# Kernel tuning notes

Hardware: AMD Instinct MI355X
Metric: run time of the kernel (lower is better)

The kernel has to match this reference:

```python
import jax, jax.numpy as jnp
import numpy as np

K = 3          # kernel size
STRIDE = 1
PAD = 1        # dilation*(K-1)//2
DIL = 1


def _bilinear_gather(x, py, px):
    """Bilinear sample x[B,C,H,W] at float coords (py,px) of shape [B,K2,Ho,Wo].
    Out-of-bounds contributions are zero (matches detectron2 DeformConv).
    Returns [B,C,K2,Ho,Wo]."""
    B, C, H, W = x.shape
    xf = x.reshape(B, C, H * W)
    y0 = jnp.floor(py)
    x0 = jnp.floor(px)
    out = jnp.zeros((B, C) + py.shape[1:], dtype=x.dtype)
    gather = jax.vmap(lambda xb, ib: xb[:, ib])  # ([C,HW],[K2,Ho,Wo])->[C,K2,Ho,Wo]
    for cy, cx in ((y0, x0), (y0, x0 + 1.0), (y0 + 1.0, x0), (y0 + 1.0, x0 + 1.0)):
        wgt = (1.0 - jnp.abs(py - cy)) * (1.0 - jnp.abs(px - cx))
        valid = (cy >= 0) & (cy <= H - 1) & (cx >= 0) & (cx <= W - 1)
        yi = jnp.clip(cy, 0, H - 1).astype(jnp.int32)
        xi = jnp.clip(cx, 0, W - 1).astype(jnp.int32)
        idx = yi * W + xi  # [B,K2,Ho,Wo]
        vals = gather(xf, idx)  # [B,C,K2,Ho,Wo]
        out = out + (wgt * valid.astype(x.dtype))[:, None] * vals
    return out


def _deform_conv(x, offset, weight):
    B, C, H, W = x.shape
    Ho = (H + 2 * PAD - (DIL * (K - 1) + 1)) // STRIDE + 1
    Wo = (W + 2 * PAD - (DIL * (K - 1) + 1)) // STRIDE + 1
    K2 = K * K
    # base sampling grid
    hs = (jnp.arange(Ho) * STRIDE - PAD).astype(x.dtype)  # [Ho]
    ws = (jnp.arange(Wo) * STRIDE - PAD).astype(x.dtype)  # [Wo]
    ky, kx = jnp.meshgrid(jnp.arange(K), jnp.arange(K), indexing='ij')
    ky = (ky.reshape(-1) * DIL).astype(x.dtype)  # [K2], row-major taps
    kx = (kx.reshape(-1) * DIL).astype(x.dtype)
    # offsets: channel 2k = dy, 2k+1 = dx for tap k
    off = offset.reshape(B, K2, 2, Ho, Wo)
    dy, dx = off[:, :, 0], off[:, :, 1]  # [B,K2,Ho,Wo]
    py = hs[None, None, :, None] + ky[None, :, None, None] + dy
    px = ws[None, None, None, :] + kx[None, :, None, None] + dx
    sampled = _bilinear_gather(x, py, px)  # [B,C,K2,Ho,Wo]
    wk = weight.reshape(weight.shape[0], C, K2)  # groups=1
    return jnp.einsum('ocK,bcKhw->bohw', wk, sampled)


def setup_inputs() -> dict:
    key = jax.random.key(0)
    k1, k2, k3 = jax.random.split(key, 3)
    B, C, H, W = 8, 256, 64, 64
    x = jax.random.normal(k1, (B, C, H, W), dtype=jnp.float32)
    offset = jax.random.normal(k2, (B, 2 * K * K, H, W), dtype=jnp.float32)
    weight = jax.random.normal(k3, (256, C, K, K), dtype=jnp.float32) * 0.02
    return {"x": x, "offset": offset, "weight": weight}


def reference(x, offset, weight):
    return _deform_conv(x, offset, weight)
```

## Files before the change

### kernel.cpp

```cpp
#include <hip/hip_runtime.h>
#include <stdint.h>


#define Bb 8
#define Cc 256
#define Hh 64
#define Ww 64
#define Pp 4096
#define Oo 256
#define NK2 9
#define NPAIR 36
#define BN 64
#define SROW 40
#define WT_BYTES (2u * 72u * 256u * 32u)

typedef __attribute__((ext_vector_type(4))) float f32x4;
typedef __attribute__((ext_vector_type(8))) short s16x8;
typedef __attribute__((ext_vector_type(4))) int   i32x4;

static __device__ __forceinline__ unsigned short f2bf(float f) {
    union { float f; uint32_t u; } v; v.f = f;
    return (unsigned short)((v.u + 0x7fffu + ((v.u >> 16) & 1u)) >> 16);
}
static __device__ __forceinline__ int imin(int a, int b) { return a < b ? a : b; }
static __device__ __forceinline__ int imax(int a, int b) { return a > b ? a : b; }

__global__ void prep_weight(const float* __restrict__ w, unsigned short* __restrict__ wt) {
    __shared__ unsigned short Lw[8][2304];
    int o0 = blockIdx.x * 8, tid = threadIdx.x;
    for (int r = 0; r < 8; r++)
        for (int i = tid; i < 2304; i += 256)
            Lw[r][i] = f2bf(w[(o0 + r) * 2304 + i]);
    __syncthreads();
    int r = tid >> 5, c32 = tid & 31;
    for (int ks = 0; ks < 72; ks++) {
        int c = (ks & 7) * 32 + c32, k2 = ks >> 3;
        wt[ks * 8192 + (o0 + r) * 32 + c32] = Lw[r][c * 9 + k2];
    }
}

__global__ void prep_x(const float* __restrict__ x, unsigned short* __restrict__ xt) {
    __shared__ unsigned short t[64][65];
    int b = blockIdx.z, c0 = blockIdx.y * 64, p0 = blockIdx.x * 64;
    int tl = threadIdx.x & 63, tg = threadIdx.x >> 6;
    #pragma unroll
    for (int r = 0; r < 16; r++) {
        int cr = r * 4 + tg;
        t[cr][tl] = f2bf(x[((size_t)(b * Cc + c0 + cr) * Pp) + p0 + tl]);
    }
    __syncthreads();
    #pragma unroll
    for (int r = 0; r < 16; r++) {
        int pr = r * 4 + tg;
        xt[((size_t)(b * Pp + p0 + pr) * Cc) + c0 + tl] = t[tl][pr];
    }
}

__global__ __launch_bounds__(512, 4)
void dcn_main(const float* __restrict__ off, const unsigned short* __restrict__ wt,
              const unsigned short* __restrict__ xt, float* __restrict__ out) {
    __shared__ __align__(16) unsigned short Sl[2][2][BN][SROW];
    __shared__ __align__(16) int   tidx[NK2][BN][4];
    __shared__ __align__(16) float twgt[NK2][BN][4];

    const int b   = blockIdx.x & 7;
    const int p0  = (blockIdx.x >> 3) * BN;
    const int tid = threadIdx.x;
    const int lane = tid & 63;
    const int wv   = tid >> 6;
    const int quad = lane >> 4;
    const int l16  = lane & 15;
    const int moff = wv * 32;

    const int px  = tid >> 3;
    const int sub = tid & 7;
    const int hh_ = sub >> 2;
    const int cc_ = (sub & 3) * 8;

    const char* xtb = (const char*)xt + (size_t)b * Pp * Cc * 2;

    for (int t = tid; t < NK2 * BN; t += 512) {
        int k2 = t >> 6, pxl = t & 63;
        int pl = p0 + pxl;
        int hh = pl >> 6, ww = pl & 63;
        int ky = k2 / 3, kx = k2 - ky * 3;
        float dy = off[((size_t)(b * 18 + 2 * k2    ) * Pp) + pl];
        float dx = off[((size_t)(b * 18 + 2 * k2 + 1) * Pp) + pl];
        float py  = (float)(hh - 1 + ky) + dy;
        float pxf = (float)(ww - 1 + kx) + dx;
        float y0f = floorf(py), x0f = floorf(pxf);
        int   y0 = (int)y0f,  x0 = (int)x0f;
        int   y1 = y0 + 1,    x1 = x0 + 1;
        float ly = py - y0f,  lx = pxf - x0f;
        float oy = 1.f - ly,  ox = 1.f - lx;
        bool vy0 = (y0 >= 0) && (y0 < Hh);
        bool vy1 = (y1 >= 0) && (y1 < Hh);
        bool vx0 = (x0 >= 0) && (x0 < Ww);
        bool vx1 = (x1 >= 0) && (x1 < Ww);
        int cy0 = imin(imax(y0, 0), Hh - 1), cy1 = imin(imax(y1, 0), Hh - 1);
        int cx0 = imin(imax(x0, 0), Ww - 1), cx1 = imin(imax(x1, 0), Ww - 1);
        tidx[k2][pxl][0] = (cy0 * Ww + cx0) * 512;  twgt[k2][pxl][0] = (vy0 && vx0) ? oy * ox : 0.f;
        tidx[k2][pxl][1] = (cy0 * Ww + cx1) * 512;  twgt[k2][pxl][1] = (vy0 && vx1) ? oy * lx : 0.f;
        tidx[k2][pxl][2] = (cy1 * Ww + cx0) * 512;  twgt[k2][pxl][2] = (vy1 && vx0) ? ly * ox : 0.f;
        tidx[k2][pxl][3] = (cy1 * Ww + cx1) * 512;  twgt[k2][pxl][3] = (vy1 && vx1) ? ly * lx : 0.f;
    }
    __syncthreads();

    int   tio[4];
    float twv[4];
    {
        i32x4 ti = *(const i32x4*)&tidx[0][px][0];
        f32x4 tw = *(const f32x4*)&twgt[0][px][0];
        #pragma unroll
        for (int t = 0; t < 4; t++) { tio[t] = ti[t]; twv[t] = tw[t]; }
    }

    auto sample_into = [&](int pr) {
        int coff = (pr & 3) * 128 + sub * 16;
        float s[8];
        #pragma unroll
        for (int j = 0; j < 8; j++) s[j] = 0.f;
        #pragma unroll
        for (int t = 0; t < 4; t++) {
            uint4 v = *(const uint4*)(xtb + tio[t] + coff);
            float wg = twv[t];
            s[0] += wg * __uint_as_float(v.x << 16);
            s[1] += wg * __uint_as_float(v.x & 0xffff0000u);
            s[2] += wg * __uint_as_float(v.y << 16);
            s[3] += wg * __uint_as_float(v.y & 0xffff0000u);
            s[4] += wg * __uint_as_float(v.z << 16);
            s[5] += wg * __uint_as_float(v.z & 0xffff0000u);
            s[6] += wg * __uint_as_float(v.w << 16);
            s[7] += wg * __uint_as_float(v.w & 0xffff0000u);
        }
        uint4 d;
        d.x = __builtin_amdgcn_perm(__float_as_uint(s[1]), __float_as_uint(s[0]), 0x07060302u);
        d.y = __builtin_amdgcn_perm(__float_as_uint(s[3]), __float_as_uint(s[2]), 0x07060302u);
        d.z = __builtin_amdgcn_perm(__float_as_uint(s[5]), __float_as_uint(s[4]), 0x07060302u);
        d.w = __builtin_amdgcn_perm(__float_as_uint(s[7]), __float_as_uint(s[6]), 0x07060302u);
        *(uint4*)&Sl[pr & 1][hh_][px][cc_] = d;
    };

    f32x4 acc[2][4];
    #pragma unroll
    for (int mt = 0; mt < 2; mt++)
        #pragma unroll
        for (int nt = 0; nt < 4; nt++) acc[mt][nt] = (f32x4){0.f, 0.f, 0.f, 0.f};

    sample_into(0);

    for (int pr = 0; pr < NPAIR; pr++) {
        __syncthreads();

        const char* wb = (const char*)wt + ((size_t)pr << 15);
        s16x8 af[2][2];
        #pragma unroll
        for (int h = 0; h < 2; h++)
            #pragma unroll
            for (int mt = 0; mt < 2; mt++)
                af[h][mt] = *(const s16x8*)(wb + h * 16384 +
                                            (moff + mt * 16 + l16) * 64 + quad * 16);

        int prn = pr + 1;
        if (prn < NPAIR) {
            if ((prn & 3) == 0) {
                int k2 = prn >> 2;
                i32x4 ti = *(const i32x4*)&tidx[k2][px][0];
                f32x4 tw = *(const f32x4*)&twgt[k2][px][0];
                #pragma unroll
                for (int t = 0; t < 4; t++) { tio[t] = ti[t]; twv[t] = tw[t]; }
            }
            sample_into(prn);
        }

        #pragma unroll
        for (int h = 0; h < 2; h++) {
            s16x8 bfr[4];
            #pragma unroll
            for (int nt = 0; nt < 4; nt++)
                bfr[nt] = *(const s16x8*)&Sl[pr & 1][h][nt * 16 + l16][quad * 8];
            #pragma unroll
            for (int mt = 0; mt < 2; mt++)
                #pragma unroll
                for (int nt = 0; nt < 4; nt++)
                    acc[mt][nt] = __builtin_amdgcn_mfma_f32_16x16x32_bf16(
                        af[h][mt], bfr[nt], acc[mt][nt], 0, 0, 0);
        }
    }

    float* op = out + ((size_t)b * Oo) * Pp + p0;
    #pragma unroll
    for (int mt = 0; mt < 2; mt++)
        #pragma unroll
        for (int nt = 0; nt < 4; nt++)
            #pragma unroll
            for (int r = 0; r < 4; r++) {
                int o_ = moff + mt * 16 + quad * 4 + r;
                int p_ = nt * 16 + l16;
                op[(size_t)o_ * Pp + p_] = acc[mt][nt][r];
            }
}

extern "C" void kernel_launch(void* const* d_in, const int* in_sizes, int n_in,
                              void* d_out, int out_size, void* d_ws, size_t ws_size,
                              hipStream_t stream) {
    (void)in_sizes; (void)n_in; (void)out_size; (void)ws_size;
    const float* x   = (const float*)d_in[0];
    const float* off = (const float*)d_in[1];
    const float* w   = (const float*)d_in[2];
    float* out = (float*)d_out;

    unsigned short* wt = (unsigned short*)d_ws;
    unsigned short* xt = (unsigned short*)((char*)d_ws + WT_BYTES);

    hipLaunchKernelGGL(prep_weight, dim3(32), dim3(256), 0, stream, w, wt);
    hipLaunchKernelGGL(prep_x, dim3(64, 4, 8), dim3(256), 0, stream, x, xt);
    hipLaunchKernelGGL(dcn_main, dim3(512), dim3(512), 0, stream, off, wt, xt, out);
}
```

Before: 165.7 us.

## Merge prep kernels and software-pipeline gathers and weight loads across MFMA

The two preprocessing kernels are fused into one launch. The x transpose now uses vectorized float4 reads and a swizzled LDS tile with 16-byte stores, and the weight prep uses 4-output blocks spread over more blocks. In the main kernel, the global gathers and weight-fragment loads for the next step are issued before the current step's MFMAs, and the bilinear reduction runs after them. Weight fragments are double-buffered in registers, which hides load latency but raises register pressure. The mask on odd bf16 lanes is also dropped, accepting tiny low-bit errors.

```diff
diff --git a/kernel.cpp b/kernel.cpp
--- a/kernel.cpp
+++ b/kernel.cpp
@@ -25,34 +25,54 @@
 static __device__ __forceinline__ int imin(int a, int b) { return a < b ? a : b; }
 static __device__ __forceinline__ int imax(int a, int b) { return a > b ? a : b; }
 
-__global__ void prep_weight(const float* __restrict__ w, unsigned short* __restrict__ wt) {
-    __shared__ unsigned short Lw[8][2304];
-    int o0 = blockIdx.x * 8, tid = threadIdx.x;
-    for (int r = 0; r < 8; r++)
-        for (int i = tid; i < 2304; i += 256)
-            Lw[r][i] = f2bf(w[(o0 + r) * 2304 + i]);
-    __syncthreads();
-    int r = tid >> 5, c32 = tid & 31;
-    for (int ks = 0; ks < 72; ks++) {
-        int c = (ks & 7) * 32 + c32, k2 = ks >> 3;
-        wt[ks * 8192 + (o0 + r) * 32 + c32] = Lw[r][c * 9 + k2];
-    }
-}
-
-__global__ void prep_x(const float* __restrict__ x, unsigned short* __restrict__ xt) {
-    __shared__ unsigned short t[64][65];
-    int b = blockIdx.z, c0 = blockIdx.y * 64, p0 = blockIdx.x * 64;
-    int tl = threadIdx.x & 63, tg = threadIdx.x >> 6;
-    #pragma unroll
-    for (int r = 0; r < 16; r++) {
-        int cr = r * 4 + tg;
-        t[cr][tl] = f2bf(x[((size_t)(b * Cc + c0 + cr) * Pp) + p0 + tl]);
-    }
-    __syncthreads();
-    #pragma unroll
-    for (int r = 0; r < 16; r++) {
-        int pr = r * 4 + tg;
-        xt[((size_t)(b * Pp + p0 + pr) * Cc) + c0 + tl] = t[tl][pr];
+__global__ __launch_bounds__(256)
+void prep(const float* __restrict__ x, const float* __restrict__ w,
+          unsigned short* __restrict__ xt, unsigned short* __restrict__ wt) {
+    __shared__ __align__(16) unsigned short L[9216];
+    const int bx = blockIdx.x, tid = threadIdx.x;
+
+    if (bx < 2048) {
+        unsigned short (*t2)[72] = (unsigned short(*)[72])L;
+        const int b = bx & 7, ti = bx >> 3;
+        const int c0 = (ti & 3) * 64, p0 = (ti >> 2) * 64;
+        #pragma unroll
+        for (int rd = 0; rd < 4; rd++) {
+            int c = (tid >> 4) + rd * 16;
+            int px4 = (tid & 15) * 4;
+            f32x4 fv = *(const f32x4*)&x[(size_t)(b * Cc + c0 + c) * Pp + p0 + px4];
+            #pragma unroll
+            for (int j = 0; j < 4; j++) {
+                int px = px4 + j;
+                int chunk = ((c >> 3) + px) & 7;
+                t2[px][chunk * 8 + (c & 7)] = f2bf(fv[j]);
+            }
+        }
+        __syncthreads();
+        #pragma unroll
+        for (int rd = 0; rd < 2; rd++) {
+            int px = (tid >> 3) + rd * 32;
+            int k = tid & 7;
+            int chunk = (k + px) & 7;
+            uint4 u = *(const uint4*)&t2[px][chunk * 8];
+            *(uint4*)&xt[(size_t)(b * Pp + p0 + px) * Cc + c0 + k * 8] = u;
+        }
+    } else {
+        const int o0 = (bx - 2048) * 4;
+        #pragma unroll
+        for (int r9 = 0; r9 < 9; r9++) {
+            int idx = r9 * 256 + tid;
+            f32x4 fv = *(const f32x4*)&w[(size_t)o0 * 2304 + (size_t)idx * 4];
+            #pragma unroll
+            for (int j = 0; j < 4; j++) L[idx * 4 + j] = f2bf(fv[j]);
+        }
+        __syncthreads();
+        #pragma unroll 4
+        for (int i = 0; i < 36; i++) {
+            int ks = i * 2 + (tid >> 7);
+            int r = (tid >> 5) & 3, c32 = tid & 31;
+            int c = (ks & 7) * 32 + c32, k2 = ks >> 3;
+            wt[(size_t)ks * 8192 + (o0 + r) * 32 + c32] = L[r * 2304 + c * 9 + k2];
+        }
     }
 }
 
@@ -108,6 +128,7 @@
 
     int   tio[4];
     float twv[4];
+    uint4 g[4];
     {
         i32x4 ti = *(const i32x4*)&tidx[0][px][0];
         f32x4 tw = *(const f32x4*)&twgt[0][px][0];
@@ -115,53 +136,40 @@
         for (int t = 0; t < 4; t++) { tio[t] = ti[t]; twv[t] = tw[t]; }
     }
 
-    auto sample_into = [&](int pr) {
-        int coff = (pr & 3) * 128 + sub * 16;
-        float s[8];
-        #pragma unroll
-        for (int j = 0; j < 8; j++) s[j] = 0.f;
-        #pragma unroll
-        for (int t = 0; t < 4; t++) {
-            uint4 v = *(const uint4*)(xtb + tio[t] + coff);
-            float wg = twv[t];
-            s[0] += wg * __uint_as_float(v.x << 16);
-            s[1] += wg * __uint_as_float(v.x & 0xffff0000u);
-            s[2] += wg * __uint_as_float(v.y << 16);
-            s[3] += wg * __uint_as_float(v.y & 0xffff0000u);
-            s[4] += wg * __uint_as_float(v.z << 16);
-            s[5] += wg * __uint_as_float(v.z & 0xffff0000u);
-            s[6] += wg * __uint_as_float(v.w << 16);
-            s[7] += wg * __uint_as_float(v.w & 0xffff0000u);
-        }
-        uint4 d;
-        d.x = __builtin_amdgcn_perm(__float_as_uint(s[1]), __float_as_uint(s[0]), 0x07060302u);
-        d.y = __builtin_amdgcn_perm(__float_as_uint(s[3]), __float_as_uint(s[2]), 0x07060302u);
-        d.z = __builtin_amdgcn_perm(__float_as_uint(s[5]), __float_as_uint(s[4]), 0x07060302u);
-        d.w = __builtin_amdgcn_perm(__float_as_uint(s[7]), __float_as_uint(s[6]), 0x07060302u);
-        *(uint4*)&Sl[pr & 1][hh_][px][cc_] = d;
-    };
-
     f32x4 acc[2][4];
     #pragma unroll
     for (int mt = 0; mt < 2; mt++)
         #pragma unroll
         for (int nt = 0; nt < 4; nt++) acc[mt][nt] = (f32x4){0.f, 0.f, 0.f, 0.f};
 
-    sample_into(0);
-
-    for (int pr = 0; pr < NPAIR; pr++) {
+    auto reduce_store = [&](int prn) {
+        float s0 = 0.f, s1 = 0.f, s2 = 0.f, s3 = 0.f, s4 = 0.f, s5 = 0.f, s6 = 0.f, s7 = 0.f;
+        #pragma unroll
+        for (int t = 0; t < 4; t++) {
+            uint4 v = g[t];
+            float wg = twv[t];
+            s0 += wg * __uint_as_float(v.x << 16);
+            s1 += wg * __uint_as_float(v.x);
+            s2 += wg * __uint_as_float(v.y << 16);
+            s3 += wg * __uint_as_float(v.y);
+            s4 += wg * __uint_as_float(v.z << 16);
+            s5 += wg * __uint_as_float(v.z);
+            s6 += wg * __uint_as_float(v.w << 16);
+            s7 += wg * __uint_as_float(v.w);
+        }
+        uint4 d;
+        d.x = __builtin_amdgcn_perm(__float_as_uint(s1), __float_as_uint(s0), 0x07060302u);
+        d.y = __builtin_amdgcn_perm(__float_as_uint(s3), __float_as_uint(s2), 0x07060302u);
+        d.z = __builtin_amdgcn_perm(__float_as_uint(s5), __float_as_uint(s4), 0x07060302u);
+        d.w = __builtin_amdgcn_perm(__float_as_uint(s7), __float_as_uint(s6), 0x07060302u);
+        *(uint4*)&Sl[prn & 1][hh_][px][cc_] = d;
+    };
+
+    s16x8 afA[2][2], afB[2][2];
+
+    auto step = [&](int pr, s16x8 (&cur)[2][2], s16x8 (&nxt)[2][2]) {
         __syncthreads();
-
-        const char* wb = (const char*)wt + ((size_t)pr << 15);
-        s16x8 af[2][2];
-        #pragma unroll
-        for (int h = 0; h < 2; h++)
-            #pragma unroll
-            for (int mt = 0; mt < 2; mt++)
-                af[h][mt] = *(const s16x8*)(wb + h * 16384 +
-                                            (moff + mt * 16 + l16) * 64 + quad * 16);
-
-        int prn = pr + 1;
+        const int prn = pr + 1;
         if (prn < NPAIR) {
             if ((prn & 3) == 0) {
                 int k2 = prn >> 2;
@@ -170,22 +178,54 @@
                 #pragma unroll
                 for (int t = 0; t < 4; t++) { tio[t] = ti[t]; twv[t] = tw[t]; }
             }
-            sample_into(prn);
-        }
-
-        #pragma unroll
-        for (int h = 0; h < 2; h++) {
-            s16x8 bfr[4];
+            const int coff = (prn & 3) * 128 + sub * 16;
+            #pragma unroll
+            for (int t = 0; t < 4; t++)
+                g[t] = *(const uint4*)(xtb + tio[t] + coff);
+            const char* wb = (const char*)wt + ((size_t)prn << 15);
+            #pragma unroll
+            for (int h = 0; h < 2; h++)
+                #pragma unroll
+                for (int mt = 0; mt < 2; mt++)
+                    nxt[h][mt] = *(const s16x8*)(wb + h * 16384 +
+                                                 (moff + mt * 16 + l16) * 64 + quad * 16);
+        }
+        s16x8 bfr[2][4];
+        const char* sb = (const char*)&Sl[pr & 1][0][0][0];
+        #pragma unroll
+        for (int h = 0; h < 2; h++)
             #pragma unroll
             for (int nt = 0; nt < 4; nt++)
-                bfr[nt] = *(const s16x8*)&Sl[pr & 1][h][nt * 16 + l16][quad * 8];
+                bfr[h][nt] = *(const s16x8*)(sb + h * (BN * SROW * 2) +
+                                             (nt * 16 + l16) * (SROW * 2) + quad * 16);
+        #pragma unroll
+        for (int h = 0; h < 2; h++)
             #pragma unroll
             for (int mt = 0; mt < 2; mt++)
                 #pragma unroll
                 for (int nt = 0; nt < 4; nt++)
                     acc[mt][nt] = __builtin_amdgcn_mfma_f32_16x16x32_bf16(
-                        af[h][mt], bfr[nt], acc[mt][nt], 0, 0, 0);
-        }
+                        cur[h][mt], bfr[h][nt], acc[mt][nt], 0, 0, 0);
+        if (prn < NPAIR) reduce_store(prn);
+    };
+
+    {
+        #pragma unroll
+        for (int t = 0; t < 4; t++)
+            g[t] = *(const uint4*)(xtb + tio[t] + sub * 16);
+        const char* wb = (const char*)wt;
+        #pragma unroll
+        for (int h = 0; h < 2; h++)
+            #pragma unroll
+            for (int mt = 0; mt < 2; mt++)
+                afA[h][mt] = *(const s16x8*)(wb + h * 16384 +
+                                             (moff + mt * 16 + l16) * 64 + quad * 16);
+        reduce_store(0);
+    }
+
+    for (int pr = 0; pr < NPAIR; pr += 2) {
+        step(pr,     afA, afB);
+        step(pr + 1, afB, afA);
     }
 
     float* op = out + ((size_t)b * Oo) * Pp + p0;
@@ -213,7 +253,6 @@
     unsigned short* wt = (unsigned short*)d_ws;
     unsigned short* xt = (unsigned short*)((char*)d_ws + WT_BYTES);
 
-    hipLaunchKernelGGL(prep_weight, dim3(32), dim3(256), 0, stream, w, wt);
-    hipLaunchKernelGGL(prep_x, dim3(64, 4, 8), dim3(256), 0, stream, x, xt);
+    hipLaunchKernelGGL(prep, dim3(2112), dim3(256), 0, stream, x, w, xt, wt);
     hipLaunchKernelGGL(dcn_main, dim3(512), dim3(512), 0, stream, off, wt, xt, out);
 }
```

Result: faster. 147.5 us (-11.0%).
